# Kernel tuning notes

Hardware: AMD Instinct MI355X
Metric: run time of the kernel (lower is better)

## Reference

```python
import jax, jax.numpy as jnp
import numpy as np

N, D, H, E = 8192, 1024, 4096, 8
LN_EPS = 1e-5


def setup_inputs() -> dict:
    key = jax.random.key(0)
    ks = jax.random.split(key, 7)
    s_in = 1.0 / np.sqrt(D)
    s_hid = 1.0 / np.sqrt(H)
    return {
        "x": jax.random.normal(ks[0], (N, D), dtype=jnp.float32),
        "gate_w": jax.random.uniform(ks[1], (E, D), jnp.float32, -s_in, s_in),
        "gate_b": jax.random.uniform(ks[2], (E,), jnp.float32, -s_in, s_in),
        "w1": jax.random.uniform(ks[3], (E, H, D), jnp.float32, -s_in, s_in),
        "b1": jax.random.uniform(ks[4], (E, H), jnp.float32, -s_in, s_in),
        "w2": jax.random.uniform(ks[5], (E, D, H), jnp.float32, -s_hid, s_hid),
        "b2": jax.random.uniform(ks[6], (E, D), jnp.float32, -s_hid, s_hid),
        "ln_w": jnp.ones((D,), jnp.float32),
        "ln_b": jnp.zeros((D,), jnp.float32),
        "top_k": 2,
    }


def reference(x, gate_w, gate_b, w1, b1, w2, b2, ln_w, ln_b, top_k):
    # Gating: softmax over experts, then top-k, then renormalizing softmax over the k scores
    gate_scores = jax.nn.softmax(x @ gate_w.T + gate_b, axis=-1)          # [N, E]
    topk_scores, topk_idx = jax.lax.top_k(gate_scores, top_k)             # [N, K]
    topk_scores = jax.nn.softmax(topk_scores, axis=-1)                    # [N, K]

    # Dense all-expert FFN (matches original: every expert runs on every token)
    h = jax.nn.relu(jnp.einsum('nd,ehd->neh', x, w1) + b1)                # [N, E, H]
    y = jnp.einsum('neh,edh->ned', h, w2) + b2                            # [N, E, D]

    # Per-token gather of the top-k expert outputs and weighted combine
    sel = jnp.take_along_axis(y, topk_idx[:, :, None], axis=1)            # [N, K, D]
    moe_out = jnp.sum(topk_scores[:, :, None] * sel, axis=1)              # [N, D]

    # Residual + LayerNorm
    r = x + moe_out
    mu = jnp.mean(r, axis=-1, keepdims=True)
    var = jnp.mean(jnp.square(r - mu), axis=-1, keepdims=True)
    return (r - mu) * jax.lax.rsqrt(var + LN_EPS) * ln_w + ln_b
```

## Files before the change

### kernel.cpp

```cpp
#include <hip/hip_runtime.h>
#include <hip/hip_bf16.h>
#include <stdint.h>

#define N_TOK 8192
#define DIM 1024
#define HID 4096
#define NEXP 8
#define NSLOT 16384
#define NBLK 64

typedef __attribute__((ext_vector_type(8))) __bf16 bf16x8;
typedef __attribute__((ext_vector_type(4))) float f32x4;

__device__ __forceinline__ unsigned short f2bf(float f) {
  unsigned int u = __float_as_uint(f);
  u += 0x7fff + ((u >> 16) & 1);
  return (unsigned short)(u >> 16);
}
__device__ __forceinline__ float bf2f(unsigned short s) {
  return __uint_as_float(((unsigned int)s) << 16);
}
__device__ __forceinline__ void async16(const void* g, void* l) {
  __builtin_amdgcn_global_load_lds((__attribute__((address_space(1))) void*)(g),
                                   (__attribute__((address_space(3))) void*)(l), 16, 0, 0);
}

__global__ void cvt_kernel(const float* __restrict__ src, unsigned short* __restrict__ dst,
                           int n4) {
  int i = blockIdx.x * 256 + threadIdx.x;
  int stride = gridDim.x * 256;
  for (; i < n4; i += stride) {
    float4 v = ((const float4*)src)[i];
    ushort4 o;
    o.x = f2bf(v.x); o.y = f2bf(v.y); o.z = f2bf(v.z); o.w = f2bf(v.w);
    ((ushort4*)dst)[i] = o;
  }
}

__global__ void gate_kernel(const float* __restrict__ x, const float* __restrict__ gw,
                            const float* __restrict__ gb, int* __restrict__ expert2,
                            float* __restrict__ score2) {
  int token = blockIdx.x * 4 + (threadIdx.x >> 6);
  int lane = threadIdx.x & 63;
  const float4* xr = (const float4*)(x + (size_t)token * DIM);
  float acc[NEXP];
#pragma unroll
  for (int e = 0; e < NEXP; ++e) acc[e] = 0.f;
#pragma unroll
  for (int it = 0; it < DIM / 4 / 64; ++it) {
    int d = it * 64 + lane;
    float4 xv = xr[d];
#pragma unroll
    for (int e = 0; e < NEXP; ++e) {
      float4 wv = ((const float4*)(gw + e * DIM))[d];
      acc[e] += xv.x * wv.x + xv.y * wv.y + xv.z * wv.z + xv.w * wv.w;
    }
  }
#pragma unroll
  for (int off = 32; off > 0; off >>= 1) {
#pragma unroll
    for (int e = 0; e < NEXP; ++e) acc[e] += __shfl_xor(acc[e], off, 64);
  }
  if (lane == 0) {
    float lg[NEXP], mx = -1e30f;
#pragma unroll
    for (int e = 0; e < NEXP; ++e) { lg[e] = acc[e] + gb[e]; mx = fmaxf(mx, lg[e]); }
    float p[NEXP], s = 0.f;
#pragma unroll
    for (int e = 0; e < NEXP; ++e) { p[e] = expf(lg[e] - mx); s += p[e]; }
    float inv = 1.f / s;
#pragma unroll
    for (int e = 0; e < NEXP; ++e) p[e] *= inv;
    int i0 = 0;
#pragma unroll
    for (int e = 1; e < NEXP; ++e) if (p[e] > p[i0]) i0 = e;
    int i1 = (i0 == 0) ? 1 : 0;
#pragma unroll
    for (int e = 0; e < NEXP; ++e) if (e != i0 && p[e] > p[i1]) i1 = e;
    float eb = expf(p[i1] - p[i0]);
    float dn = 1.f / (1.f + eb);
    expert2[token * 2] = i0;
    expert2[token * 2 + 1] = i1;
    score2[token * 2] = dn;
    score2[token * 2 + 1] = eb * dn;
  }
}

__global__ void hist_kernel(const int* __restrict__ expert2, int* __restrict__ hist) {
  __shared__ int lh[NEXP];
  int b = blockIdx.x, t = threadIdx.x;
  if (t < NEXP) lh[t] = 0;
  __syncthreads();
  atomicAdd(&lh[expert2[b * 256 + t]], 1);
  __syncthreads();
  if (t < NEXP) hist[b * NEXP + t] = lh[t];
}

__global__ void scan_kernel(const int* __restrict__ hist, int* __restrict__ cnt,
                            int* __restrict__ off_, int* __restrict__ base) {
  __shared__ int lh[NBLK * NEXP];
  __shared__ int ltot[NEXP];
  __shared__ int loff[NEXP];
  int t = threadIdx.x;
#pragma unroll
  for (int e = 0; e < NEXP; ++e) lh[t * NEXP + e] = hist[t * NEXP + e];
  __syncthreads();
  if (t < NEXP) {
    int s = 0;
    for (int b = 0; b < NBLK; ++b) { int v = lh[b * NEXP + t]; lh[b * NEXP + t] = s; s += v; }
    ltot[t] = s;
  }
  __syncthreads();
  if (t == 0) {
    int s = 0;
#pragma unroll
    for (int e = 0; e < NEXP; ++e) { loff[e] = s; s += ltot[e]; }
  }
  __syncthreads();
  if (t < NEXP) { cnt[t] = ltot[t]; off_[t] = loff[t]; }
#pragma unroll
  for (int e = 0; e < NEXP; ++e) base[t * NEXP + e] = loff[e] + lh[t * NEXP + e];
}

__global__ void assign_kernel(const int* __restrict__ expert2, const int* __restrict__ base,
                              int* __restrict__ slot_of, int* __restrict__ token_of) {
  __shared__ int lh[NEXP];
  int b = blockIdx.x, t = threadIdx.x;
  if (t < NEXP) lh[t] = 0;
  __syncthreads();
  int i = b * 256 + t;
  int e = expert2[i];
  int r = atomicAdd(&lh[e], 1);
  int slot = base[b * NEXP + e] + r;
  slot_of[i] = slot;
  token_of[slot] = i >> 1;
}

__global__ void gather_kernel(const float* __restrict__ x, const int* __restrict__ token_of,
                              unsigned short* __restrict__ xg) {
  int slot = blockIdx.x;
  int t = threadIdx.x;
  int n = token_of[slot];
  float4 v = *(const float4*)(x + (size_t)n * DIM + t * 4);
  ushort4 o;
  o.x = f2bf(v.x); o.y = f2bf(v.y); o.z = f2bf(v.z); o.w = f2bf(v.w);
  *(ushort4*)(xg + (size_t)slot * DIM + t * 4) = o;
}

template <int KLEN, int NLEN, bool RELU, bool BCVT>
__global__ __launch_bounds__(256, 4) void gemm_bt(
    const unsigned short* __restrict__ A, const void* __restrict__ Bptr,
    const float* __restrict__ bias, unsigned short* __restrict__ C,
    const int* __restrict__ cnt, const int* __restrict__ off_) {
  const int NB_N = NLEN / 128;
  int panel = blockIdx.z * 8 + blockIdx.x;
  int e = panel / NB_N;
  int n0 = (panel % NB_N) * 128;
  int me = cnt[e];
  int m0 = blockIdx.y * 128;
  if (m0 >= me) return;
  int rb = off_[e] + m0;

  __shared__ unsigned short lA[8192];
  __shared__ unsigned short lB[8192];

  int tid = threadIdx.x;
  int wave = tid >> 6, lane = tid & 63;
  int wm = (wave >> 1) * 64, wn = (wave & 1) * 64;
  int quad = lane >> 4, l16 = lane & 15;
  int x7 = l16 & 7;

  int arow[4], brow[4], akx[4], ldst[4];
#pragma unroll
  for (int i = 0; i < 4; ++i) {
    int c = i * 256 + tid;
    int row = c >> 3;
    akx[i] = (c & 7) ^ (row & 7);
    ldst[i] = c * 8;
    brow[i] = row;
    int grow = rb + row;
    arow[i] = (grow > NSLOT - 1) ? (NSLOT - 1) : grow;
  }

  f32x4 acc[4][4];
#pragma unroll
  for (int i = 0; i < 4; ++i)
#pragma unroll
    for (int j = 0; j < 4; ++j) acc[i][j] = {0.f, 0.f, 0.f, 0.f};

  const unsigned short* Bb = (const unsigned short*)Bptr + (size_t)e * NLEN * KLEN;
  const float* Bf = (const float*)Bptr + (size_t)e * NLEN * KLEN;

  for (int k0 = 0; k0 < KLEN; k0 += 64) {
#pragma unroll
    for (int i = 0; i < 4; ++i)
      async16(A + (size_t)arow[i] * KLEN + k0 + akx[i] * 8, &lA[ldst[i]]);
    if (BCVT) {
#pragma unroll
      for (int i = 0; i < 4; ++i)
        async16(Bb + (size_t)(n0 + brow[i]) * KLEN + k0 + akx[i] * 8, &lB[ldst[i]]);
    } else {
#pragma unroll
      for (int i = 0; i < 4; ++i) {
        const float* gp = Bf + (size_t)(n0 + brow[i]) * KLEN + k0 + akx[i] * 8;
        float4 v0 = *(const float4*)gp;
        float4 v1 = *(const float4*)(gp + 4);
        union { unsigned short u[8]; bf16x8 v; } pk;
        pk.u[0] = f2bf(v0.x); pk.u[1] = f2bf(v0.y); pk.u[2] = f2bf(v0.z); pk.u[3] = f2bf(v0.w);
        pk.u[4] = f2bf(v1.x); pk.u[5] = f2bf(v1.y); pk.u[6] = f2bf(v1.z); pk.u[7] = f2bf(v1.w);
        *(bf16x8*)(&lB[ldst[i]]) = pk.v;
      }
    }
    __syncthreads();
#pragma unroll
    for (int s = 0; s < 2; ++s) {
      int qx = (s * 4 + quad) ^ x7;
      bf16x8 af[4], bfr[4];
#pragma unroll
      for (int mt = 0; mt < 4; ++mt)
        af[mt] = *(const bf16x8*)(&lA[(wm + mt * 16 + l16) * 64 + qx * 8]);
#pragma unroll
      for (int nt = 0; nt < 4; ++nt)
        bfr[nt] = *(const bf16x8*)(&lB[(wn + nt * 16 + l16) * 64 + qx * 8]);
#pragma unroll
      for (int mt = 0; mt < 4; ++mt)
#pragma unroll
        for (int nt = 0; nt < 4; ++nt)
          acc[mt][nt] =
              __builtin_amdgcn_mfma_f32_16x16x32_bf16(af[mt], bfr[nt], acc[mt][nt], 0, 0, 0);
    }
    __syncthreads();
  }
#pragma unroll
  for (int mt = 0; mt < 4; ++mt) {
#pragma unroll
    for (int r = 0; r < 4; ++r) {
      int mrow = wm + mt * 16 + quad * 4 + r;
      if (m0 + mrow < me) {
#pragma unroll
        for (int nt = 0; nt < 4; ++nt) {
          int col = n0 + wn + nt * 16 + l16;
          float v = acc[mt][nt][r] + bias[e * NLEN + col];
          if (RELU) v = fmaxf(v, 0.f);
          C[(size_t)(rb + mrow) * NLEN + col] = f2bf(v);
        }
      }
    }
  }
}

__global__ void ln_kernel(const float* __restrict__ x, const unsigned short* __restrict__ y,
                          const int* __restrict__ slot_of, const float* __restrict__ score2,
                          const float* __restrict__ lnw, const float* __restrict__ lnb,
                          float* __restrict__ out) {
  __shared__ float red[8];
  int n = blockIdx.x, t = threadIdx.x;
  int wave = t >> 6, lane = t & 63;
  int s0 = slot_of[n * 2], s1 = slot_of[n * 2 + 1];
  float w0 = score2[n * 2], w1 = score2[n * 2 + 1];
  float4 xv = *(const float4*)(x + (size_t)n * DIM + t * 4);
  ushort4 y0 = *(const ushort4*)(y + (size_t)s0 * DIM + t * 4);
  ushort4 y1 = *(const ushort4*)(y + (size_t)s1 * DIM + t * 4);
  float r0 = xv.x + w0 * bf2f(y0.x) + w1 * bf2f(y1.x);
  float r1 = xv.y + w0 * bf2f(y0.y) + w1 * bf2f(y1.y);
  float r2 = xv.z + w0 * bf2f(y0.z) + w1 * bf2f(y1.z);
  float r3 = xv.w + w0 * bf2f(y0.w) + w1 * bf2f(y1.w);
  float sum = r0 + r1 + r2 + r3;
  float sq = r0 * r0 + r1 * r1 + r2 * r2 + r3 * r3;
#pragma unroll
  for (int off = 32; off > 0; off >>= 1) {
    sum += __shfl_xor(sum, off, 64);
    sq += __shfl_xor(sq, off, 64);
  }
  if (lane == 0) { red[wave] = sum; red[4 + wave] = sq; }
  __syncthreads();
  sum = red[0] + red[1] + red[2] + red[3];
  sq = red[4] + red[5] + red[6] + red[7];
  float mu = sum * (1.f / DIM);
  float var = sq * (1.f / DIM) - mu * mu;
  float rs = rsqrtf(var + 1e-5f);
  float4 wv = *(const float4*)(lnw + t * 4);
  float4 bv = *(const float4*)(lnb + t * 4);
  float4 o;
  o.x = (r0 - mu) * rs * wv.x + bv.x;
  o.y = (r1 - mu) * rs * wv.y + bv.y;
  o.z = (r2 - mu) * rs * wv.z + bv.z;
  o.w = (r3 - mu) * rs * wv.w + bv.w;
  *(float4*)(out + (size_t)n * DIM + t * 4) = o;
}

extern "C" void kernel_launch(void* const* d_in, const int* in_sizes, int n_in,
                              void* d_out, int out_size, void* d_ws, size_t ws_size,
                              hipStream_t stream) {
  const float* x = (const float*)d_in[0];
  const float* gw = (const float*)d_in[1];
  const float* gb = (const float*)d_in[2];
  const float* w1 = (const float*)d_in[3];
  const float* b1 = (const float*)d_in[4];
  const float* w2 = (const float*)d_in[5];
  const float* b2 = (const float*)d_in[6];
  const float* lnw = (const float*)d_in[7];
  const float* lnb = (const float*)d_in[8];
  float* out = (float*)d_out;
  char* ws = (char*)d_ws;

  int* cnt = (int*)(ws + 0);
  int* off_ = (int*)(ws + 64);
  int* hist = (int*)(ws + 4096);
  int* base = (int*)(ws + 4096 + 2048);
  int* expert2 = (int*)(ws + 65536);
  float* score2 = (float*)(ws + 2 * 65536);
  int* slot_of = (int*)(ws + 3 * 65536);
  int* token_of = (int*)(ws + 4 * 65536);
  const size_t XG_OFF = 524288;
  const size_t H_OFF = XG_OFF + (size_t)NSLOT * DIM * 2;
  const size_t Y_OFF = H_OFF + (size_t)NSLOT * HID * 2;
  const size_t WB1_OFF = Y_OFF + (size_t)NSLOT * DIM * 2;
  const size_t WB2_OFF = WB1_OFF + (size_t)NEXP * HID * DIM * 2;
  const size_t WS_NEED = WB2_OFF + (size_t)NEXP * DIM * HID * 2;
  unsigned short* xg = (unsigned short*)(ws + XG_OFF);
  unsigned short* h = (unsigned short*)(ws + H_OFF);
  unsigned short* y = (unsigned short*)(ws + Y_OFF);
  unsigned short* wb1 = (unsigned short*)(ws + WB1_OFF);
  unsigned short* wb2 = (unsigned short*)(ws + WB2_OFF);
  bool cvt_ok = ws_size >= WS_NEED;

  gate_kernel<<<N_TOK / 4, 256, 0, stream>>>(x, gw, gb, expert2, score2);
  hist_kernel<<<NBLK, 256, 0, stream>>>(expert2, hist);
  scan_kernel<<<1, 64, 0, stream>>>(hist, cnt, off_, base);
  assign_kernel<<<NBLK, 256, 0, stream>>>(expert2, base, slot_of, token_of);
  gather_kernel<<<NSLOT, 256, 0, stream>>>(x, token_of, xg);
  if (cvt_ok) {
    const int n4 = NEXP * HID * DIM / 4;
    cvt_kernel<<<4096, 256, 0, stream>>>(w1, wb1, n4);
    cvt_kernel<<<4096, 256, 0, stream>>>(w2, wb2, n4);
    gemm_bt<DIM, HID, true, true>
        <<<dim3(8, 128, (NEXP * HID / 128) / 8), 256, 0, stream>>>(xg, wb1, b1, h, cnt, off_);
    gemm_bt<HID, DIM, false, true>
        <<<dim3(8, 128, (NEXP * DIM / 128) / 8), 256, 0, stream>>>(h, wb2, b2, y, cnt, off_);
  } else {
    gemm_bt<DIM, HID, true, false>
        <<<dim3(8, 128, (NEXP * HID / 128) / 8), 256, 0, stream>>>(xg, w1, b1, h, cnt, off_);
    gemm_bt<HID, DIM, false, false>
        <<<dim3(8, 128, (NEXP * DIM / 128) / 8), 256, 0, stream>>>(h, w2, b2, y, cnt, off_);
  }
  ln_kernel<<<N_TOK, 256, 0, stream>>>(x, y, slot_of, score2, lnw, lnb, out);
}
```

Before: 757.5 us.

## Add 256x256 double-buffered pipelined grouped GEMM for bf16 expert weights

Adds a 512-thread gemm256 kernel with 256x256 output tiles, double-buffered LDS staging via async global-to-LDS loads, interleaved half-tile prefetches, explicit waitcnt/barriers and s_setprio around MFMA bursts. It replaces the 128x128 single-buffered gemm_bt on the path where weights were pre-converted to bf16. The larger tile raises arithmetic intensity and the pipelining is meant to hide load latency behind MFMA work. The cost is 128KB of LDS and high register use per block, which limits occupancy, plus more wasted work on partially filled expert tiles.

```diff
diff --git a/kernel.cpp b/kernel.cpp
--- a/kernel.cpp
+++ b/kernel.cpp
@@ -24,6 +24,7 @@
   __builtin_amdgcn_global_load_lds((__attribute__((address_space(1))) void*)(g),
                                    (__attribute__((address_space(3))) void*)(l), 16, 0, 0);
 }
+#define MFMA16(a, b, c) __builtin_amdgcn_mfma_f32_16x16x32_bf16(a, b, c, 0, 0, 0)
 
 __global__ void cvt_kernel(const float* __restrict__ src, unsigned short* __restrict__ dst,
                            int n4) {
@@ -147,7 +148,158 @@
   *(ushort4*)(xg + (size_t)slot * DIM + t * 4) = o;
 }
 
-template <int KLEN, int NLEN, bool RELU, bool BCVT>
+template <int KLEN, int NLEN, bool RELU>
+__global__ __launch_bounds__(512, 2) void gemm256(
+    const unsigned short* __restrict__ A, const unsigned short* __restrict__ B,
+    const float* __restrict__ bias, unsigned short* __restrict__ C,
+    const int* __restrict__ cnt, const int* __restrict__ off_) {
+  const int NB_N = NLEN / 256;
+  const int NT = KLEN / 64;
+  int panel = blockIdx.z * 8 + blockIdx.x;
+  int e = panel / NB_N;
+  int n0 = (panel % NB_N) * 256;
+  int me = cnt[e];
+  int m0 = blockIdx.y * 256;
+  if (m0 >= me) return;
+  int rb = off_[e] + m0;
+
+  __shared__ unsigned short lA[2][16384];
+  __shared__ unsigned short lB[2][16384];
+
+  int tid = threadIdx.x;
+  int wave = tid >> 6, lane = tid & 63;
+  int wm = wave >> 2, wn = wave & 3;
+  int quad = lane >> 4, l16 = lane & 15;
+  int x7 = l16 & 7;
+
+  int crow = tid >> 3, kc = tid & 7;
+  int sslot = kc ^ (crow & 7);
+  const char* Ab = (const char*)A;
+  const char* Bbb = (const char*)(B + (size_t)e * NLEN * KLEN);
+  int a0r = rb + crow;       a0r = a0r > NSLOT - 1 ? NSLOT - 1 : a0r;
+  int a1r = rb + 64 + crow;  a1r = a1r > NSLOT - 1 ? NSLOT - 1 : a1r;
+  int a2r = rb + 128 + crow; a2r = a2r > NSLOT - 1 ? NSLOT - 1 : a2r;
+  int a3r = rb + 192 + crow; a3r = a3r > NSLOT - 1 ? NSLOT - 1 : a3r;
+  uint32_t aof0 = (uint32_t)a0r * (KLEN * 2) + sslot * 16;
+  uint32_t aof1 = (uint32_t)a1r * (KLEN * 2) + sslot * 16;
+  uint32_t aof2 = (uint32_t)a2r * (KLEN * 2) + sslot * 16;
+  uint32_t aof3 = (uint32_t)a3r * (KLEN * 2) + sslot * 16;
+  uint32_t bof0 = (uint32_t)(n0 + crow) * (KLEN * 2) + sslot * 16;
+  uint32_t bof1 = bof0 + 64 * (KLEN * 2);
+  uint32_t bof2 = bof0 + 128 * (KLEN * 2);
+  uint32_t bof3 = bof0 + 192 * (KLEN * 2);
+  const int d0 = tid * 8, d1 = (512 + tid) * 8, d2 = (1024 + tid) * 8, d3 = (1536 + tid) * 8;
+
+#define STG_A0(p, kb) { async16(Ab + aof0 + (kb), &lA[p][d0]); async16(Ab + aof1 + (kb), &lA[p][d1]); }
+#define STG_A1(p, kb) { async16(Ab + aof2 + (kb), &lA[p][d2]); async16(Ab + aof3 + (kb), &lA[p][d3]); }
+#define STG_B0(p, kb) { async16(Bbb + bof0 + (kb), &lB[p][d0]); async16(Bbb + bof1 + (kb), &lB[p][d1]); }
+#define STG_B1(p, kb) { async16(Bbb + bof2 + (kb), &lB[p][d2]); async16(Bbb + bof3 + (kb), &lB[p][d3]); }
+
+  f32x4 acc[8][4];
+#pragma unroll
+  for (int i = 0; i < 8; ++i)
+#pragma unroll
+    for (int j = 0; j < 4; ++j) acc[i][j] = {0.f, 0.f, 0.f, 0.f};
+
+  STG_A0(0, 0); STG_A1(0, 0); STG_B0(0, 0); STG_B1(0, 0);
+  STG_A0(1, 128); STG_B0(1, 128);
+  asm volatile("s_waitcnt vmcnt(4)" ::: "memory");
+  __builtin_amdgcn_sched_barrier(0);
+  __builtin_amdgcn_s_barrier();
+
+  const int abase = (wm * 128 + l16) * 64;
+  const int bbase = (wn * 64 + l16) * 64;
+  const int s0off = (quad ^ x7) * 8;
+  const int s1off = ((4 + quad) ^ x7) * 8;
+
+#pragma unroll 2
+  for (int t = 0; t < NT; ++t) {
+    const int p = t & 1;
+    const unsigned short* pA = lA[p];
+    const unsigned short* pB = lB[p];
+    const int kb1 = t * 128 + 128;
+    bf16x8 a0lo[4], a0hi[4], a1[8], b0[4], b1[4];
+#pragma unroll
+    for (int mt = 0; mt < 4; ++mt) a0lo[mt] = *(const bf16x8*)&pA[abase + mt * 1024 + s0off];
+#pragma unroll
+    for (int nt = 0; nt < 4; ++nt) b0[nt] = *(const bf16x8*)&pB[bbase + nt * 1024 + s0off];
+    if (t + 1 < NT) STG_A1(p ^ 1, kb1);
+    __builtin_amdgcn_s_barrier();
+    asm volatile("s_waitcnt lgkmcnt(0)" ::: "memory");
+    __builtin_amdgcn_sched_barrier(0);
+    __builtin_amdgcn_s_setprio(1);
+#pragma unroll
+    for (int mt = 0; mt < 4; ++mt)
+#pragma unroll
+      for (int nt = 0; nt < 4; ++nt) acc[mt][nt] = MFMA16(a0lo[mt], b0[nt], acc[mt][nt]);
+    __builtin_amdgcn_s_setprio(0);
+    __builtin_amdgcn_s_barrier();
+#pragma unroll
+    for (int mt = 0; mt < 4; ++mt) a0hi[mt] = *(const bf16x8*)&pA[abase + (4 + mt) * 1024 + s0off];
+#pragma unroll
+    for (int mt = 0; mt < 8; ++mt) a1[mt] = *(const bf16x8*)&pA[abase + mt * 1024 + s1off];
+#pragma unroll
+    for (int nt = 0; nt < 4; ++nt) b1[nt] = *(const bf16x8*)&pB[bbase + nt * 1024 + s1off];
+    if (t + 1 < NT) STG_B1(p ^ 1, kb1);
+    __builtin_amdgcn_s_barrier();
+    asm volatile("s_waitcnt lgkmcnt(0)" ::: "memory");
+    __builtin_amdgcn_sched_barrier(0);
+    __builtin_amdgcn_s_setprio(1);
+#pragma unroll
+    for (int mt = 0; mt < 4; ++mt)
+#pragma unroll
+      for (int nt = 0; nt < 4; ++nt) acc[4 + mt][nt] = MFMA16(a0hi[mt], b0[nt], acc[4 + mt][nt]);
+    __builtin_amdgcn_s_setprio(0);
+    __builtin_amdgcn_s_barrier();
+    if (t + 2 < NT) STG_A0(p, kb1 + 128);
+    __builtin_amdgcn_s_barrier();
+    __builtin_amdgcn_s_setprio(1);
+#pragma unroll
+    for (int mt = 0; mt < 4; ++mt)
+#pragma unroll
+      for (int nt = 0; nt < 4; ++nt) acc[mt][nt] = MFMA16(a1[mt], b1[nt], acc[mt][nt]);
+    __builtin_amdgcn_s_setprio(0);
+    __builtin_amdgcn_s_barrier();
+    if (t + 2 < NT) STG_B0(p, kb1 + 128);
+    __builtin_amdgcn_s_barrier();
+    __builtin_amdgcn_s_setprio(1);
+#pragma unroll
+    for (int mt = 0; mt < 4; ++mt)
+#pragma unroll
+      for (int nt = 0; nt < 4; ++nt) acc[4 + mt][nt] = MFMA16(a1[4 + mt], b1[nt], acc[4 + mt][nt]);
+    __builtin_amdgcn_s_setprio(0);
+    if (t + 2 < NT) {
+      asm volatile("s_waitcnt vmcnt(4)" ::: "memory");
+    } else {
+      asm volatile("s_waitcnt vmcnt(0)" ::: "memory");
+    }
+    __builtin_amdgcn_sched_barrier(0);
+    __builtin_amdgcn_s_barrier();
+  }
+#undef STG_A0
+#undef STG_A1
+#undef STG_B0
+#undef STG_B1
+
+#pragma unroll
+  for (int mt = 0; mt < 8; ++mt) {
+#pragma unroll
+    for (int r = 0; r < 4; ++r) {
+      int mrow = wm * 128 + mt * 16 + quad * 4 + r;
+      if (m0 + mrow < me) {
+#pragma unroll
+        for (int nt = 0; nt < 4; ++nt) {
+          int col = n0 + wn * 64 + nt * 16 + l16;
+          float v = acc[mt][nt][r] + bias[e * NLEN + col];
+          if (RELU) v = fmaxf(v, 0.f);
+          C[(size_t)(rb + mrow) * NLEN + col] = f2bf(v);
+        }
+      }
+    }
+  }
+}
+
+template <int KLEN, int NLEN, bool RELU>
 __global__ __launch_bounds__(256, 4) void gemm_bt(
     const unsigned short* __restrict__ A, const void* __restrict__ Bptr,
     const float* __restrict__ bias, unsigned short* __restrict__ C,
@@ -188,28 +340,21 @@
 #pragma unroll
     for (int j = 0; j < 4; ++j) acc[i][j] = {0.f, 0.f, 0.f, 0.f};
 
-  const unsigned short* Bb = (const unsigned short*)Bptr + (size_t)e * NLEN * KLEN;
   const float* Bf = (const float*)Bptr + (size_t)e * NLEN * KLEN;
 
   for (int k0 = 0; k0 < KLEN; k0 += 64) {
 #pragma unroll
     for (int i = 0; i < 4; ++i)
       async16(A + (size_t)arow[i] * KLEN + k0 + akx[i] * 8, &lA[ldst[i]]);
-    if (BCVT) {
-#pragma unroll
-      for (int i = 0; i < 4; ++i)
-        async16(Bb + (size_t)(n0 + brow[i]) * KLEN + k0 + akx[i] * 8, &lB[ldst[i]]);
-    } else {
-#pragma unroll
-      for (int i = 0; i < 4; ++i) {
-        const float* gp = Bf + (size_t)(n0 + brow[i]) * KLEN + k0 + akx[i] * 8;
-        float4 v0 = *(const float4*)gp;
-        float4 v1 = *(const float4*)(gp + 4);
-        union { unsigned short u[8]; bf16x8 v; } pk;
-        pk.u[0] = f2bf(v0.x); pk.u[1] = f2bf(v0.y); pk.u[2] = f2bf(v0.z); pk.u[3] = f2bf(v0.w);
-        pk.u[4] = f2bf(v1.x); pk.u[5] = f2bf(v1.y); pk.u[6] = f2bf(v1.z); pk.u[7] = f2bf(v1.w);
-        *(bf16x8*)(&lB[ldst[i]]) = pk.v;
-      }
+#pragma unroll
+    for (int i = 0; i < 4; ++i) {
+      const float* gp = Bf + (size_t)(n0 + brow[i]) * KLEN + k0 + akx[i] * 8;
+      float4 v0 = *(const float4*)gp;
+      float4 v1 = *(const float4*)(gp + 4);
+      union { unsigned short u[8]; bf16x8 v; } pk;
+      pk.u[0] = f2bf(v0.x); pk.u[1] = f2bf(v0.y); pk.u[2] = f2bf(v0.z); pk.u[3] = f2bf(v0.w);
+      pk.u[4] = f2bf(v1.x); pk.u[5] = f2bf(v1.y); pk.u[6] = f2bf(v1.z); pk.u[7] = f2bf(v1.w);
+      *(bf16x8*)(&lB[ldst[i]]) = pk.v;
     }
     __syncthreads();
 #pragma unroll
@@ -226,8 +371,7 @@
       for (int mt = 0; mt < 4; ++mt)
 #pragma unroll
         for (int nt = 0; nt < 4; ++nt)
-          acc[mt][nt] =
-              __builtin_amdgcn_mfma_f32_16x16x32_bf16(af[mt], bfr[nt], acc[mt][nt], 0, 0, 0);
+          acc[mt][nt] = MFMA16(af[mt], bfr[nt], acc[mt][nt]);
     }
     __syncthreads();
   }
@@ -334,14 +478,14 @@
     const int n4 = NEXP * HID * DIM / 4;
     cvt_kernel<<<4096, 256, 0, stream>>>(w1, wb1, n4);
     cvt_kernel<<<4096, 256, 0, stream>>>(w2, wb2, n4);
-    gemm_bt<DIM, HID, true, true>
-        <<<dim3(8, 128, (NEXP * HID / 128) / 8), 256, 0, stream>>>(xg, wb1, b1, h, cnt, off_);
-    gemm_bt<HID, DIM, false, true>
-        <<<dim3(8, 128, (NEXP * DIM / 128) / 8), 256, 0, stream>>>(h, wb2, b2, y, cnt, off_);
+    gemm256<DIM, HID, true>
+        <<<dim3(8, 64, (NEXP * HID / 256) / 8), 512, 0, stream>>>(xg, wb1, b1, h, cnt, off_);
+    gemm256<HID, DIM, false>
+        <<<dim3(8, 64, (NEXP * DIM / 256) / 8), 512, 0, stream>>>(h, wb2, b2, y, cnt, off_);
   } else {
-    gemm_bt<DIM, HID, true, false>
+    gemm_bt<DIM, HID, true>
         <<<dim3(8, 128, (NEXP * HID / 128) / 8), 256, 0, stream>>>(xg, w1, b1, h, cnt, off_);
-    gemm_bt<HID, DIM, false, false>
+    gemm_bt<HID, DIM, false>
         <<<dim3(8, 128, (NEXP * DIM / 128) / 8), 256, 0, stream>>>(h, w2, b2, y, cnt, off_);
   }
   ln_kernel<<<N_TOK, 256, 0, stream>>>(x, y, slot_of, score2, lnw, lnb, out);
```

New measurement: 1.174 ms. +55.0%, slower.

## Double-buffer LDS tiles in bf16 expert GEMMs to overlap loads with MFMA

Applied to the files above, without the earlier changes.

Adds a gemm_p2 kernel for the pre-converted bf16 weight path that keeps two LDS buffers for A and B tiles. The next k-tile is loaded asynchronously while the MFMAs run on the current one, with a single waitcnt and barrier per iteration instead of two syncthreads. This doubles LDS use per block and lowers launch_bounds occupancy from 4 to 2 blocks per CU, trading occupancy-based latency hiding for explicit prefetch.

```diff
diff --git a/kernel.cpp b/kernel.cpp
--- a/kernel.cpp
+++ b/kernel.cpp
@@ -24,6 +24,7 @@
   __builtin_amdgcn_global_load_lds((__attribute__((address_space(1))) void*)(g),
                                    (__attribute__((address_space(3))) void*)(l), 16, 0, 0);
 }
+#define MFMA16(a, b, c) __builtin_amdgcn_mfma_f32_16x16x32_bf16(a, b, c, 0, 0, 0)
 
 __global__ void cvt_kernel(const float* __restrict__ src, unsigned short* __restrict__ dst,
                            int n4) {
@@ -147,7 +148,107 @@
   *(ushort4*)(xg + (size_t)slot * DIM + t * 4) = o;
 }
 
-template <int KLEN, int NLEN, bool RELU, bool BCVT>
+template <int KLEN, int NLEN, bool RELU>
+__global__ __launch_bounds__(256, 2) void gemm_p2(
+    const unsigned short* __restrict__ A, const unsigned short* __restrict__ B,
+    const float* __restrict__ bias, unsigned short* __restrict__ C,
+    const int* __restrict__ cnt, const int* __restrict__ off_) {
+  const int NB_N = NLEN / 128;
+  int panel = blockIdx.z * 8 + blockIdx.x;
+  int e = panel / NB_N;
+  int n0 = (panel % NB_N) * 128;
+  int me = cnt[e];
+  int m0 = blockIdx.y * 128;
+  if (m0 >= me) return;
+  int rb = off_[e] + m0;
+
+  __shared__ unsigned short lA[2][8192];
+  __shared__ unsigned short lB[2][8192];
+
+  int tid = threadIdx.x;
+  int wave = tid >> 6, lane = tid & 63;
+  int wm = (wave >> 1) * 64, wn = (wave & 1) * 64;
+  int quad = lane >> 4, l16 = lane & 15;
+  int x7 = l16 & 7;
+
+  int arow[4], brow[4], akx[4], ldst[4];
+#pragma unroll
+  for (int i = 0; i < 4; ++i) {
+    int c = i * 256 + tid;
+    int row = c >> 3;
+    akx[i] = (c & 7) ^ (row & 7);
+    ldst[i] = c * 8;
+    brow[i] = row;
+    int grow = rb + row;
+    arow[i] = (grow > NSLOT - 1) ? (NSLOT - 1) : grow;
+  }
+
+  const unsigned short* Bb = B + (size_t)e * NLEN * KLEN;
+
+#define STAGE(buf, kof)                                                          \
+  {                                                                              \
+    _Pragma("unroll") for (int i = 0; i < 4; ++i)                                \
+        async16(A + (size_t)arow[i] * KLEN + (kof) + akx[i] * 8, &lA[buf][ldst[i]]); \
+    _Pragma("unroll") for (int i = 0; i < 4; ++i)                                \
+        async16(Bb + (size_t)(n0 + brow[i]) * KLEN + (kof) + akx[i] * 8,         \
+                &lB[buf][ldst[i]]);                                              \
+  }
+
+  f32x4 acc[4][4];
+#pragma unroll
+  for (int i = 0; i < 4; ++i)
+#pragma unroll
+    for (int j = 0; j < 4; ++j) acc[i][j] = {0.f, 0.f, 0.f, 0.f};
+
+  STAGE(0, 0);
+  asm volatile("s_waitcnt vmcnt(0)" ::: "memory");
+  __builtin_amdgcn_sched_barrier(0);
+  __builtin_amdgcn_s_barrier();
+
+  for (int k0 = 0; k0 < KLEN; k0 += 64) {
+    const int cur = (k0 >> 6) & 1;
+    if (k0 + 64 < KLEN) STAGE(cur ^ 1, k0 + 64);
+#pragma unroll
+    for (int s = 0; s < 2; ++s) {
+      int qx = (s * 4 + quad) ^ x7;
+      bf16x8 af[4], bfr[4];
+#pragma unroll
+      for (int mt = 0; mt < 4; ++mt)
+        af[mt] = *(const bf16x8*)(&lA[cur][(wm + mt * 16 + l16) * 64 + qx * 8]);
+#pragma unroll
+      for (int nt = 0; nt < 4; ++nt)
+        bfr[nt] = *(const bf16x8*)(&lB[cur][(wn + nt * 16 + l16) * 64 + qx * 8]);
+#pragma unroll
+      for (int mt = 0; mt < 4; ++mt)
+#pragma unroll
+        for (int nt = 0; nt < 4; ++nt)
+          acc[mt][nt] = MFMA16(af[mt], bfr[nt], acc[mt][nt]);
+    }
+    asm volatile("s_waitcnt vmcnt(0)" ::: "memory");
+    __builtin_amdgcn_sched_barrier(0);
+    __builtin_amdgcn_s_barrier();
+  }
+#undef STAGE
+
+#pragma unroll
+  for (int mt = 0; mt < 4; ++mt) {
+#pragma unroll
+    for (int r = 0; r < 4; ++r) {
+      int mrow = wm + mt * 16 + quad * 4 + r;
+      if (m0 + mrow < me) {
+#pragma unroll
+        for (int nt = 0; nt < 4; ++nt) {
+          int col = n0 + wn + nt * 16 + l16;
+          float v = acc[mt][nt][r] + bias[e * NLEN + col];
+          if (RELU) v = fmaxf(v, 0.f);
+          C[(size_t)(rb + mrow) * NLEN + col] = f2bf(v);
+        }
+      }
+    }
+  }
+}
+
+template <int KLEN, int NLEN, bool RELU>
 __global__ __launch_bounds__(256, 4) void gemm_bt(
     const unsigned short* __restrict__ A, const void* __restrict__ Bptr,
     const float* __restrict__ bias, unsigned short* __restrict__ C,
@@ -188,28 +289,21 @@
 #pragma unroll
     for (int j = 0; j < 4; ++j) acc[i][j] = {0.f, 0.f, 0.f, 0.f};
 
-  const unsigned short* Bb = (const unsigned short*)Bptr + (size_t)e * NLEN * KLEN;
   const float* Bf = (const float*)Bptr + (size_t)e * NLEN * KLEN;
 
   for (int k0 = 0; k0 < KLEN; k0 += 64) {
 #pragma unroll
     for (int i = 0; i < 4; ++i)
       async16(A + (size_t)arow[i] * KLEN + k0 + akx[i] * 8, &lA[ldst[i]]);
-    if (BCVT) {
-#pragma unroll
-      for (int i = 0; i < 4; ++i)
-        async16(Bb + (size_t)(n0 + brow[i]) * KLEN + k0 + akx[i] * 8, &lB[ldst[i]]);
-    } else {
-#pragma unroll
-      for (int i = 0; i < 4; ++i) {
-        const float* gp = Bf + (size_t)(n0 + brow[i]) * KLEN + k0 + akx[i] * 8;
-        float4 v0 = *(const float4*)gp;
-        float4 v1 = *(const float4*)(gp + 4);
-        union { unsigned short u[8]; bf16x8 v; } pk;
-        pk.u[0] = f2bf(v0.x); pk.u[1] = f2bf(v0.y); pk.u[2] = f2bf(v0.z); pk.u[3] = f2bf(v0.w);
-        pk.u[4] = f2bf(v1.x); pk.u[5] = f2bf(v1.y); pk.u[6] = f2bf(v1.z); pk.u[7] = f2bf(v1.w);
-        *(bf16x8*)(&lB[ldst[i]]) = pk.v;
-      }
+#pragma unroll
+    for (int i = 0; i < 4; ++i) {
+      const float* gp = Bf + (size_t)(n0 + brow[i]) * KLEN + k0 + akx[i] * 8;
+      float4 v0 = *(const float4*)gp;
+      float4 v1 = *(const float4*)(gp + 4);
+      union { unsigned short u[8]; bf16x8 v; } pk;
+      pk.u[0] = f2bf(v0.x); pk.u[1] = f2bf(v0.y); pk.u[2] = f2bf(v0.z); pk.u[3] = f2bf(v0.w);
+      pk.u[4] = f2bf(v1.x); pk.u[5] = f2bf(v1.y); pk.u[6] = f2bf(v1.z); pk.u[7] = f2bf(v1.w);
+      *(bf16x8*)(&lB[ldst[i]]) = pk.v;
     }
     __syncthreads();
 #pragma unroll
@@ -226,8 +320,7 @@
       for (int mt = 0; mt < 4; ++mt)
 #pragma unroll
         for (int nt = 0; nt < 4; ++nt)
-          acc[mt][nt] =
-              __builtin_amdgcn_mfma_f32_16x16x32_bf16(af[mt], bfr[nt], acc[mt][nt], 0, 0, 0);
+          acc[mt][nt] = MFMA16(af[mt], bfr[nt], acc[mt][nt]);
     }
     __syncthreads();
   }
@@ -334,14 +427,14 @@
     const int n4 = NEXP * HID * DIM / 4;
     cvt_kernel<<<4096, 256, 0, stream>>>(w1, wb1, n4);
     cvt_kernel<<<4096, 256, 0, stream>>>(w2, wb2, n4);
-    gemm_bt<DIM, HID, true, true>
+    gemm_p2<DIM, HID, true>
         <<<dim3(8, 128, (NEXP * HID / 128) / 8), 256, 0, stream>>>(xg, wb1, b1, h, cnt, off_);
-    gemm_bt<HID, DIM, false, true>
+    gemm_p2<HID, DIM, false>
         <<<dim3(8, 128, (NEXP * DIM / 128) / 8), 256, 0, stream>>>(h, wb2, b2, y, cnt, off_);
   } else {
-    gemm_bt<DIM, HID, true, false>
+    gemm_bt<DIM, HID, true>
         <<<dim3(8, 128, (NEXP * HID / 128) / 8), 256, 0, stream>>>(xg, w1, b1, h, cnt, off_);
-    gemm_bt<HID, DIM, false, false>
+    gemm_bt<HID, DIM, false>
         <<<dim3(8, 128, (NEXP * DIM / 128) / 8), 256, 0, stream>>>(h, w2, b2, y, cnt, off_);
   }
   ln_kernel<<<N_TOK, 256, 0, stream>>>(x, y, slot_of, score2, lnw, lnb, out);
```

New measurement: 895.1 us. 18.2% more time.
